# Optimization experiments

Measured on AMD Instinct MI355X. Metric: run time of the kernel, lower is better.

The kernel has to match this reference:

```python
import jax, jax.numpy as jnp
import numpy as np

TAU = 2.0
EPS_COH = 1e-8
EPS_NLL = 1e-7
ALPHA = 0.0
# component-vs-modality mask: rows = (common, synergy, g_spec, p_spec), cols = (gene, path)
MASK = np.array([[1.0, 1.0], [0.0, 0.0], [1.0, 0.0], [0.0, 1.0]], dtype=np.float32)


def l2norm(x, axis=-1):
    n = jnp.sqrt(jnp.sum(x * x, axis=axis, keepdims=True))
    return x / jnp.maximum(n, 1e-12)


def setup_inputs() -> dict:
    key = jax.random.key(0)
    ks = jax.random.split(key, 8)
    B, K, C, N = 64, 4, 256, 8192
    hazards = jax.random.uniform(ks[0], (B, K), dtype=jnp.float32)
    S = jnp.cumprod(1.0 - hazards, axis=1)  # survival curve, matches torch semantics
    indiv = jax.random.normal(ks[1], (B, 4, C), dtype=jnp.float32)
    gene = jax.random.normal(ks[2], (B, 1, C), dtype=jnp.float32)
    path = jax.random.normal(ks[3], (B, 1, C), dtype=jnp.float32)
    cohort_bank = jax.random.normal(ks[4], (K, N, 4, C), dtype=jnp.float32)
    label = jax.random.randint(ks[5], (B,), 0, K).astype(jnp.int32)
    c = jax.random.randint(ks[6], (B,), 0, 2).astype(jnp.int32)
    return {"hazards": hazards, "S": S, "indiv": indiv, "gene": gene,
            "path": path, "cohort_bank": cohort_bank, "label": label, "c": c}


def reference(hazards, S, indiv, gene, path, cohort_bank, label, c):
    B, K = hazards.shape
    dt = hazards.dtype
    # ---- NLLSurvLoss ----
    cf = c.astype(dt)[:, None]                       # [B,1] censoring flag
    Y = label.astype(jnp.int32)[:, None]             # [B,1]
    S_padded = jnp.concatenate([jnp.ones((B, 1), dt), S], axis=1)  # [B,K+1]
    s_y = jnp.take_along_axis(S_padded, Y, axis=1)
    h_y = jnp.take_along_axis(hazards, Y, axis=1)
    s_y1 = jnp.take_along_axis(S_padded, Y + 1, axis=1)
    clamp = lambda x: jnp.maximum(x, EPS_NLL)
    uncensored = -(1.0 - cf) * (jnp.log(clamp(s_y)) + jnp.log(clamp(h_y)))
    censored = -cf * jnp.log(clamp(s_y1))
    neg_l = censored + uncensored
    nll = ((1.0 - ALPHA) * neg_l + ALPHA * uncensored).mean()
    # ---- CohortLoss: intra ----
    indiv_n = l2norm(indiv)                          # [B,4,C]
    gp_n = l2norm(jnp.concatenate([gene, path], axis=1))  # [B,2,C]
    sim = jnp.einsum('bpc,btc->bpt', indiv_n, gp_n)  # [B,4,2]
    mask = jnp.asarray(MASK, dtype=dt)               # [4,2]
    intra = (jnp.abs(sim) * (1.0 - mask) - mask * sim).mean(axis=(1, 2)) + 1.0
    intra_loss = intra.mean()
    # ---- CohortLoss: inter (vectorized cohort-bank retrieval) ----
    n_cls, N = cohort_bank.shape[0], cohort_bank.shape[1]
    anchors = l2norm(indiv.mean(axis=1))             # [B,C]
    bank_means = cohort_bank.mean(axis=2)            # [n_cls,N,C]
    bank_n = l2norm(bank_means)                      # [n_cls,N,C]
    sims = jnp.einsum('knc,bc->bkn', bank_n, anchors)  # [B,n_cls,N]
    e = jnp.exp(sims / TAU)
    pos_mask = (label[:, None] == jnp.arange(n_cls, dtype=label.dtype)[None, :]).astype(dt)[:, :, None]  # [B,n_cls,1]
    ep = jnp.sum(e * pos_mask) / (B * N)                       # mean over B*N positive sims
    en = jnp.sum(e * (1.0 - pos_mask)) / (B * (n_cls - 1) * N)  # mean over B*(n_cls-1)*N negative sims
    inter_loss = -jnp.log((ep + EPS_COH) / (ep + en + EPS_COH))
    cohort_loss = intra_loss + inter_loss
    # Loss_factory: total = 1.0*nllsurv + 1.0*cohort
    return nll + cohort_loss
```

## Files before the change

kernel.cpp:

```cpp
#include <hip/hip_runtime.h>
#include <math.h>

#define BB 64
#define KK 4
#define CC 256
#define NN 8192
#define NROWS (KK*NN)
#define GRID_INTER 512
#define WPG 4
#define TILES (GRID_INTER*WPG)

#define WS_B_OFF     0
#define WS_SLOT_OFF  32768
#define WS_NLL_OFF   40960
#define WS_INTRA_OFF 41216
#define WS_TKT_OFF   41472

#define EPS_NLL 1e-7f

typedef __attribute__((ext_vector_type(8))) short bf16x8;
typedef __attribute__((ext_vector_type(4))) float f32x4;

__device__ __forceinline__ float4 f4add(float4 a, float4 b){ return make_float4(a.x+b.x, a.y+b.y, a.z+b.z, a.w+b.w); }
__device__ __forceinline__ float4 f4scale(float4 a, float s){ return make_float4(a.x*s, a.y*s, a.z*s, a.w*s); }
__device__ __forceinline__ float dot4(float4 a, float4 b){ return a.x*b.x + a.y*b.y + a.z*b.z + a.w*b.w; }

__device__ __forceinline__ float wred(float v){
#pragma unroll
  for (int m = 32; m >= 1; m >>= 1) v += __shfl_xor(v, m, 64);
  return v;
}

__device__ __forceinline__ unsigned short f2bf(float x){
  union { float f; unsigned u; } v; v.f = x;
  unsigned r = v.u + 0x7fffu + ((v.u >> 16) & 1u);
  return (unsigned short)(r >> 16);
}

__global__ __launch_bounds__(64) void prep_kernel(
    const float* __restrict__ hazards, const float* __restrict__ S,
    const float* __restrict__ indiv,   const float* __restrict__ gene,
    const float* __restrict__ path,    const int* __restrict__ label,
    const int* __restrict__ cvec,      char* __restrict__ ws)
{
  const int b = blockIdx.x;
  const int lane = threadIdx.x;

  const float4* ind4 = (const float4*)indiv + (size_t)b * 256;
  float4 i0 = ind4[  0 + lane];
  float4 i1 = ind4[ 64 + lane];
  float4 i2 = ind4[128 + lane];
  float4 i3 = ind4[192 + lane];
  float4 g  = ((const float4*)gene)[b*64 + lane];
  float4 p  = ((const float4*)path)[b*64 + lane];

  float4 am = f4scale(f4add(f4add(i0, i1), f4add(i2, i3)), 0.25f);
  float na = sqrtf(wred(dot4(am, am)));
  float4 an = f4scale(am, 1.0f / fmaxf(na, 1e-12f));

  {
    const int cq = lane;
    const unsigned addr = (unsigned)((cq >> 3) * 4096
                        + (b >> 4) * 1024
                        + ((((cq >> 1) & 3) * 16) + (b & 15)) * 16
                        + (cq & 1) * 8);
    ushort4 h4;
    h4.x = f2bf(an.x); h4.y = f2bf(an.y); h4.z = f2bf(an.z); h4.w = f2bf(an.w);
    *(ushort4*)(ws + WS_B_OFF + addr) = h4;
  }

  float4 v[6] = {i0, i1, i2, i3, g, p};
#pragma unroll
  for (int j = 0; j < 6; ++j) {
    float n = sqrtf(wred(dot4(v[j], v[j])));
    v[j] = f4scale(v[j], 1.0f / fmaxf(n, 1e-12f));
  }

  float s[4][2];
#pragma unroll
  for (int pp = 0; pp < 4; ++pp)
#pragma unroll
    for (int t = 0; t < 2; ++t)
      s[pp][t] = wred(dot4(v[pp], v[4+t]));

  if (lane == 0) {
    float intra = (-s[0][0]) + (-s[0][1])
                + fabsf(s[1][0]) + fabsf(s[1][1])
                + (-s[2][0]) + fabsf(s[2][1])
                + fabsf(s[3][0]) + (-s[3][1]);
    intra = intra * 0.125f + 1.0f;
    ((float*)(ws + WS_INTRA_OFF))[b] = intra;

    int   Y  = label[b];
    float cf = (float)cvec[b];
    float s_y  = (Y == 0) ? 1.0f : S[b*KK + Y - 1];
    float s_y1 = S[b*KK + Y];
    float h_y  = hazards[b*KK + Y];
    float neg_l = -cf * logf(fmaxf(s_y1, EPS_NLL))
                  - (1.0f - cf) * (logf(fmaxf(s_y, EPS_NLL)) + logf(fmaxf(h_y, EPS_NLL)));
    ((float*)(ws + WS_NLL_OFF))[b] = neg_l;
  }
}

__global__ __launch_bounds__(256) void inter_kernel(
    const float* __restrict__ bank, const int* __restrict__ label,
    char* __restrict__ ws, float* __restrict__ out)
{
  __shared__ uint4 Bl[2048];
  __shared__ double redw[WPG][2];
  __shared__ unsigned tkt_s;

  const int tid  = threadIdx.x;
  const int wave = tid >> 6;
  const int lane = tid & 63;
  const int lm   = lane & 15;
  const int lg   = lane >> 4;

  const uint4* Bg = (const uint4*)(ws + WS_B_OFF);
#pragma unroll
  for (int i = 0; i < 8; ++i) Bl[tid + i*256] = Bg[tid + i*256];
  __syncthreads();

  const int gw   = blockIdx.x * WPG + wave;
  const int row0 = gw * 16;
  const int kk   = row0 >> 13;

  int lab[4];
#pragma unroll
  for (int nt = 0; nt < 4; ++nt) lab[nt] = label[nt*16 + lm];

  const float* rp = bank + (size_t)(row0 + lm) * 1024 + lg * 8;

  float4 sA[8][2];
#pragma unroll
  for (int kc = 0; kc < 8; ++kc)
#pragma unroll
    for (int p = 0; p < 2; ++p)
      sA[kc][p] = *(const float4*)(rp + kc*32 + p*4);
#pragma unroll
  for (int c = 1; c < 4; ++c)
#pragma unroll
    for (int kc = 0; kc < 8; ++kc)
#pragma unroll
      for (int p = 0; p < 2; ++p) {
        float4 t = *(const float4*)(rp + c*256 + kc*32 + p*4);
        sA[kc][p] = f4add(sA[kc][p], t);
      }

  float ss = 0.0f;
#pragma unroll
  for (int kc = 0; kc < 8; ++kc)
#pragma unroll
    for (int p = 0; p < 2; ++p)
      ss += dot4(sA[kc][p], sA[kc][p]);
  ss += __shfl_xor(ss, 16, 64);
  ss += __shfl_xor(ss, 32, 64);
  const float rs = rsqrtf(fmaxf(ss, 1e-24f));

  f32x4 acc0 = {0,0,0,0}, acc1 = {0,0,0,0}, acc2 = {0,0,0,0}, acc3 = {0,0,0,0};
#pragma unroll
  for (int kc = 0; kc < 8; ++kc) {
    float4 u = sA[kc][0], v = sA[kc][1];
    bf16x8 a;
    a[0] = (short)f2bf(u.x*rs); a[1] = (short)f2bf(u.y*rs);
    a[2] = (short)f2bf(u.z*rs); a[3] = (short)f2bf(u.w*rs);
    a[4] = (short)f2bf(v.x*rs); a[5] = (short)f2bf(v.y*rs);
    a[6] = (short)f2bf(v.z*rs); a[7] = (short)f2bf(v.w*rs);
    acc0 = __builtin_amdgcn_mfma_f32_16x16x32_bf16(a, *(const bf16x8*)&Bl[(kc*4+0)*64 + lane], acc0, 0, 0, 0);
    acc1 = __builtin_amdgcn_mfma_f32_16x16x32_bf16(a, *(const bf16x8*)&Bl[(kc*4+1)*64 + lane], acc1, 0, 0, 0);
    acc2 = __builtin_amdgcn_mfma_f32_16x16x32_bf16(a, *(const bf16x8*)&Bl[(kc*4+2)*64 + lane], acc2, 0, 0, 0);
    acc3 = __builtin_amdgcn_mfma_f32_16x16x32_bf16(a, *(const bf16x8*)&Bl[(kc*4+3)*64 + lane], acc3, 0, 0, 0);
  }

  float epf = 0.0f, enf = 0.0f;
#define DO_NT(ACC, NT)                                                        \
  {                                                                           \
    float es = expf(ACC.x * 0.5f) + expf(ACC.y * 0.5f)                        \
             + expf(ACC.z * 0.5f) + expf(ACC.w * 0.5f);                       \
    if (lab[NT] == kk) epf += es; else enf += es;                             \
  }
  DO_NT(acc0, 0) DO_NT(acc1, 1) DO_NT(acc2, 2) DO_NT(acc3, 3)
#undef DO_NT

  epf = wred(epf);
  enf = wred(enf);
  if (lane == 0) {
    redw[wave][0] = (double)epf;
    redw[wave][1] = (double)enf;
  }
  __syncthreads();

  double*   slots  = (double*)(ws + WS_SLOT_OFF);
  unsigned* ticket = (unsigned*)(ws + WS_TKT_OFF);

  if (tid == 0) {
    double bep = 0.0, ben = 0.0;
#pragma unroll
    for (int w = 0; w < WPG; ++w) { bep += redw[w][0]; ben += redw[w][1]; }
    slots[blockIdx.x*2 + 0] = bep;
    slots[blockIdx.x*2 + 1] = ben;
    __threadfence();
    tkt_s = atomicAdd(ticket, 1u);
  }
  __syncthreads();

  if (tkt_s == GRID_INTER - 1 && wave == 0) {
    __threadfence();
    double pep = 0.0, pen = 0.0;
    for (int i = lane; i < GRID_INTER; i += 64) {
      pep += slots[2*i + 0];
      pen += slots[2*i + 1];
    }
#pragma unroll
    for (int m = 32; m >= 1; m >>= 1) {
      pep += __shfl_xor(pep, m, 64);
      pen += __shfl_xor(pen, m, 64);
    }
    float scal = ((const float*)(ws + WS_NLL_OFF))[lane]
               + ((const float*)(ws + WS_INTRA_OFF))[lane];
    scal = wred(scal);
    if (lane == 0) {
      double ep = pep / (double)(BB * NN);
      double en = pen / (double)(BB * (KK-1) * NN);
      double inter = -log((ep + 1e-8) / (ep + en + 1e-8));
      out[0] = (float)((double)scal / 64.0 + inter);
    }
  }
}

extern "C" void kernel_launch(void* const* d_in, const int* in_sizes, int n_in,
                              void* d_out, int out_size, void* d_ws, size_t ws_size,
                              hipStream_t stream)
{
  const float* hazards = (const float*)d_in[0];
  const float* S       = (const float*)d_in[1];
  const float* indiv   = (const float*)d_in[2];
  const float* gene    = (const float*)d_in[3];
  const float* path    = (const float*)d_in[4];
  const float* bank    = (const float*)d_in[5];
  const int*   label   = (const int*)d_in[6];
  const int*   cvec    = (const int*)d_in[7];
  char*  ws  = (char*)d_ws;
  float* out = (float*)d_out;

  hipMemsetAsync(ws + WS_TKT_OFF, 0, 4, stream);
  prep_kernel<<<dim3(BB), dim3(64), 0, stream>>>(hazards, S, indiv, gene, path, label, cvec, ws);
  inter_kernel<<<dim3(GRID_INTER), dim3(256), 0, stream>>>(bank, label, ws, out);
}
```

Measured before the change: 235.3 us.

## Split bank mean-normalization into a separate coalesced bf16 pre-pass kernel

Adds a bank_norm_kernel that reads the fp32 cohort bank with fully coalesced float4 loads, averages the 4 components, L2-normalizes, and writes bf16 rows to the workspace. The inter kernel then loads these compact bf16 rows directly as MFMA operands instead of reducing fp32 data in registers. This is meant to cut the register pressure and the poorly coalesced strided loads in the main kernel. The cost is an extra kernel launch and a 16 MB intermediate write and read.

```diff
diff --git a/kernel.cpp b/kernel.cpp
--- a/kernel.cpp
+++ b/kernel.cpp
@@ -6,15 +6,16 @@
 #define CC 256
 #define NN 8192
 #define NROWS (KK*NN)
+#define GRID_NORM 2048
 #define GRID_INTER 512
 #define WPG 4
-#define TILES (GRID_INTER*WPG)
-
-#define WS_B_OFF     0
-#define WS_SLOT_OFF  32768
-#define WS_NLL_OFF   40960
-#define WS_INTRA_OFF 41216
-#define WS_TKT_OFF   41472
+
+#define WS_BN_OFF    0
+#define WS_B_OFF     16777216
+#define WS_SLOT_OFF  16809984
+#define WS_NLL_OFF   16818176
+#define WS_INTRA_OFF 16818432
+#define WS_TKT_OFF   16818688
 
 #define EPS_NLL 1e-7f
 
@@ -102,9 +103,39 @@
   }
 }
 
+__global__ __launch_bounds__(256, 4) void bank_norm_kernel(
+    const float* __restrict__ bank, char* __restrict__ ws)
+{
+  const int tid  = threadIdx.x;
+  const int wave = tid >> 6;
+  const int lane = tid & 63;
+  const int gw   = blockIdx.x * WPG + wave;
+  const int row0 = gw * 4;
+
+  const float4* b4 = (const float4*)bank;
+  ushort4* bn = (ushort4*)(ws + WS_BN_OFF);
+
+  float4 r[4][4];
+#pragma unroll
+  for (int rr = 0; rr < 4; ++rr)
+#pragma unroll
+    for (int c = 0; c < 4; ++c)
+      r[rr][c] = b4[(size_t)(row0 + rr) * 256 + c * 64 + lane];
+
+#pragma unroll
+  for (int rr = 0; rr < 4; ++rr) {
+    float4 m = f4add(f4add(r[rr][0], r[rr][1]), f4add(r[rr][2], r[rr][3]));
+    float ss = wred(dot4(m, m));
+    float rs = rsqrtf(fmaxf(ss, 1e-24f));
+    ushort4 h4;
+    h4.x = f2bf(m.x * rs); h4.y = f2bf(m.y * rs);
+    h4.z = f2bf(m.z * rs); h4.w = f2bf(m.w * rs);
+    bn[(size_t)(row0 + rr) * 64 + lane] = h4;
+  }
+}
+
 __global__ __launch_bounds__(256) void inter_kernel(
-    const float* __restrict__ bank, const int* __restrict__ label,
-    char* __restrict__ ws, float* __restrict__ out)
+    const int* __restrict__ label, char* __restrict__ ws, float* __restrict__ out)
 {
   __shared__ uint4 Bl[2048];
   __shared__ double redw[WPG][2];
@@ -129,47 +160,19 @@
 #pragma unroll
   for (int nt = 0; nt < 4; ++nt) lab[nt] = label[nt*16 + lm];
 
-  const float* rp = bank + (size_t)(row0 + lm) * 1024 + lg * 8;
-
-  float4 sA[8][2];
+  const short* bnp = (const short*)(ws + WS_BN_OFF) + (size_t)(row0 + lm) * 256 + lg * 8;
+  bf16x8 af[8];
 #pragma unroll
   for (int kc = 0; kc < 8; ++kc)
-#pragma unroll
-    for (int p = 0; p < 2; ++p)
-      sA[kc][p] = *(const float4*)(rp + kc*32 + p*4);
-#pragma unroll
-  for (int c = 1; c < 4; ++c)
-#pragma unroll
-    for (int kc = 0; kc < 8; ++kc)
-#pragma unroll
-      for (int p = 0; p < 2; ++p) {
-        float4 t = *(const float4*)(rp + c*256 + kc*32 + p*4);
-        sA[kc][p] = f4add(sA[kc][p], t);
-      }
-
-  float ss = 0.0f;
-#pragma unroll
-  for (int kc = 0; kc < 8; ++kc)
-#pragma unroll
-    for (int p = 0; p < 2; ++p)
-      ss += dot4(sA[kc][p], sA[kc][p]);
-  ss += __shfl_xor(ss, 16, 64);
-  ss += __shfl_xor(ss, 32, 64);
-  const float rs = rsqrtf(fmaxf(ss, 1e-24f));
+    af[kc] = *(const bf16x8*)(bnp + kc * 32);
 
   f32x4 acc0 = {0,0,0,0}, acc1 = {0,0,0,0}, acc2 = {0,0,0,0}, acc3 = {0,0,0,0};
 #pragma unroll
   for (int kc = 0; kc < 8; ++kc) {
-    float4 u = sA[kc][0], v = sA[kc][1];
-    bf16x8 a;
-    a[0] = (short)f2bf(u.x*rs); a[1] = (short)f2bf(u.y*rs);
-    a[2] = (short)f2bf(u.z*rs); a[3] = (short)f2bf(u.w*rs);
-    a[4] = (short)f2bf(v.x*rs); a[5] = (short)f2bf(v.y*rs);
-    a[6] = (short)f2bf(v.z*rs); a[7] = (short)f2bf(v.w*rs);
-    acc0 = __builtin_amdgcn_mfma_f32_16x16x32_bf16(a, *(const bf16x8*)&Bl[(kc*4+0)*64 + lane], acc0, 0, 0, 0);
-    acc1 = __builtin_amdgcn_mfma_f32_16x16x32_bf16(a, *(const bf16x8*)&Bl[(kc*4+1)*64 + lane], acc1, 0, 0, 0);
-    acc2 = __builtin_amdgcn_mfma_f32_16x16x32_bf16(a, *(const bf16x8*)&Bl[(kc*4+2)*64 + lane], acc2, 0, 0, 0);
-    acc3 = __builtin_amdgcn_mfma_f32_16x16x32_bf16(a, *(const bf16x8*)&Bl[(kc*4+3)*64 + lane], acc3, 0, 0, 0);
+    acc0 = __builtin_amdgcn_mfma_f32_16x16x32_bf16(af[kc], *(const bf16x8*)&Bl[(kc*4+0)*64 + lane], acc0, 0, 0, 0);
+    acc1 = __builtin_amdgcn_mfma_f32_16x16x32_bf16(af[kc], *(const bf16x8*)&Bl[(kc*4+1)*64 + lane], acc1, 0, 0, 0);
+    acc2 = __builtin_amdgcn_mfma_f32_16x16x32_bf16(af[kc], *(const bf16x8*)&Bl[(kc*4+2)*64 + lane], acc2, 0, 0, 0);
+    acc3 = __builtin_amdgcn_mfma_f32_16x16x32_bf16(af[kc], *(const bf16x8*)&Bl[(kc*4+3)*64 + lane], acc3, 0, 0, 0);
   }
 
   float epf = 0.0f, enf = 0.0f;
@@ -245,5 +248,6 @@
 
   hipMemsetAsync(ws + WS_TKT_OFF, 0, 4, stream);
   prep_kernel<<<dim3(BB), dim3(64), 0, stream>>>(hazards, S, indiv, gene, path, label, cvec, ws);
-  inter_kernel<<<dim3(GRID_INTER), dim3(256), 0, stream>>>(bank, label, ws, out);
-}
+  bank_norm_kernel<<<dim3(GRID_NORM), dim3(256), 0, stream>>>(bank, ws);
+  inter_kernel<<<dim3(GRID_INTER), dim3(256), 0, stream>>>(label, ws, out);
+}
```

Result: faster. 229.7 us (-2.4%).
